# Optimization experiments

Measured on AMD Instinct MI355X. Metric: run time of the kernel, lower is better.

The kernel has to match this reference:

```python
import jax, jax.numpy as jnp
import numpy as np

B, G, D, H, L, MLP = 64, 512, 384, 6, 12, 4
DH = D // H
MASK_RATIO = 0.6
KEEP_RATIO = 0.1
PAD_VAL = -1.0
START_VAL = 1.0
POS_HID = 128
NEG = -1e9


def setup_inputs() -> dict:
    key = jax.random.key(0)
    ks = jax.random.split(key, 24)
    s = 0.02
    inp = {
        "x": jax.random.normal(ks[0], (B, G, D), jnp.float32),
        "center_points": jax.random.normal(ks[1], (B, G, 3), jnp.float32),
        "mask_noise": jax.random.uniform(ks[2], (B, G), jnp.float32),
        # pos embedder MLP: 3 -> 128 -> D
        "pos_w1": jax.random.normal(ks[3], (3, POS_HID), jnp.float32) * s,
        "pos_b1": jnp.zeros((POS_HID,), jnp.float32),
        "pos_w2": jax.random.normal(ks[4], (POS_HID, D), jnp.float32) * s,
        "pos_b2": jnp.zeros((D,), jnp.float32),
        # stacked per-layer transformer params
        "ln1_w": jnp.ones((L, D), jnp.float32),
        "ln1_b": jnp.zeros((L, D), jnp.float32),
        "qkv_w": jax.random.normal(ks[5], (L, D, 3 * D), jnp.float32) * s,
        "qkv_b": jnp.zeros((L, 3 * D), jnp.float32),
        "proj_w": jax.random.normal(ks[6], (L, D, D), jnp.float32) * s,
        "proj_b": jnp.zeros((L, D), jnp.float32),
        "ln2_w": jnp.ones((L, D), jnp.float32),
        "ln2_b": jnp.zeros((L, D), jnp.float32),
        "fc1_w": jax.random.normal(ks[7], (L, D, MLP * D), jnp.float32) * s,
        "fc1_b": jnp.zeros((L, MLP * D), jnp.float32),
        "fc2_w": jax.random.normal(ks[8], (L, MLP * D, D), jnp.float32) * s,
        "fc2_b": jnp.zeros((L, D), jnp.float32),
        # final LayerNorm
        "norm_w": jnp.ones((D,), jnp.float32),
        "norm_b": jnp.zeros((D,), jnp.float32),
    }
    return inp


def _layer_norm(h, w, b, eps=1e-5):
    mu = jnp.mean(h, axis=-1, keepdims=True)
    var = jnp.mean(jnp.square(h - mu), axis=-1, keepdims=True)
    return (h - mu) * jax.lax.rsqrt(var + eps) * w + b


def _random_mask(center, noise):
    # padding tokens: all coords equal PAD_VAL
    pad = jnp.all(center == PAD_VAL, axis=-1)                      # [B, G] bool
    if MASK_RATIO == 0:
        return jnp.zeros(pad.shape, bool), pad
    n = (G - jnp.sum(pad.astype(jnp.int32), axis=-1))              # non-padding count
    k = (n.astype(jnp.float32) * KEEP_RATIO).astype(jnp.int32)     # kept-first tokens
    m = ((n - k).astype(jnp.float32) * MASK_RATIO).astype(jnp.int32)
    M = jnp.max(m)
    j = jnp.arange(G)[None, :]
    # shuffle region [k, n): pick m random slots (uniform subset via rank of noise)
    region = (j >= k[:, None]) & (j < n[:, None])
    u = jnp.where(region, noise, jnp.inf)
    rank = jnp.argsort(jnp.argsort(u, axis=-1), axis=-1)
    shuf = (rank < m[:, None]) & region
    # tail of ones: positions [n, n + M - m)
    tail = (j >= n[:, None]) & (j < (n + M - m)[:, None])
    return shuf | tail, pad


def _attention(h, qw, qb, pw, pb, bias):
    qkv = (h @ qw + qb).reshape(B, G, 3, H, DH).transpose(2, 0, 3, 1, 4)
    q, k, v = qkv[0], qkv[1], qkv[2]                               # [B, H, G, DH]
    s = jnp.einsum('bhqd,bhkd->bhqk', q, k) * (DH ** -0.5) + bias
    a = jax.nn.softmax(s, axis=-1)
    o = jnp.einsum('bhqk,bhkd->bhqd', a, v).transpose(0, 2, 1, 3).reshape(B, G, D)
    return o @ pw + pb


def _forward(x, center_points, mask_noise,
             pos_w1, pos_b1, pos_w2, pos_b2,
             ln1_w, ln1_b, qkv_w, qkv_b, proj_w, proj_b,
             ln2_w, ln2_b, fc1_w, fc1_b, fc2_w, fc2_b,
             norm_w, norm_b):
    # shift right + start token
    start = jnp.full((B, 1, D), START_VAL, x.dtype)
    x = jnp.concatenate([start, x[:, :-1, :]], axis=1)
    # positional embedding of shifted centers + start-token pos
    pos = jax.nn.gelu(center_points[:, :-1, :] @ pos_w1 + pos_b1, approximate=False) @ pos_w2 + pos_b2
    pos = jnp.concatenate([jnp.full((B, 1, D), START_VAL, x.dtype), pos], axis=1)
    # causal | (random column mask & ~eye) attention mask
    triu = jnp.triu(jnp.ones((G, G), bool), 1)
    rand_mask, pad = _random_mask(center_points, mask_noise)
    eye = jnp.eye(G, dtype=bool)
    attn_mask = triu[None, :, :] | (rand_mask[:, None, :] & ~eye[None, :, :])   # [B, G, G]
    bias = jnp.where(attn_mask | pad[:, None, :], NEG, 0.0)[:, None, :, :]      # [B,1,G,G]

    def block(h, p):
        l1w, l1b, qw, qb, pw, pb, l2w, l2b, f1w, f1b, f2w, f2b = p
        h = h + pos
        h = h + _attention(_layer_norm(h, l1w, l1b), qw, qb, pw, pb, bias)
        h = h + (jax.nn.gelu(_layer_norm(h, l2w, l2b) @ f1w + f1b, approximate=False) @ f2w + f2b)
        return h, None

    x, _ = jax.lax.scan(block, x, (ln1_w, ln1_b, qkv_w, qkv_b, proj_w, proj_b,
                                   ln2_w, ln2_b, fc1_w, fc1_b, fc2_w, fc2_b))
    x = _layer_norm(x, norm_w, norm_b)
    return x, pad, attn_mask


def reference(x, center_points, mask_noise,
              pos_w1, pos_b1, pos_w2, pos_b2,
              ln1_w, ln1_b, qkv_w, qkv_b, proj_w, proj_b,
              ln2_w, ln2_b, fc1_w, fc1_b, fc2_w, fc2_b,
              norm_w, norm_b):
    out, pad, attn_mask = _forward(x, center_points, mask_noise,
                                   pos_w1, pos_b1, pos_w2, pos_b2,
                                   ln1_w, ln1_b, qkv_w, qkv_b, proj_w, proj_b,
                                   ln2_w, ln2_b, fc1_w, fc1_b, fc2_w, fc2_b,
                                   norm_w, norm_b)
    # torch repeat_interleave over heads -> [B*H, G, G]
    return out, pad, jnp.repeat(attn_mask, H, axis=0)
```

## Files before the change

### kernel.cpp

```cpp
#include <hip/hip_runtime.h>
#include <math.h>

typedef _Float16 f16;
typedef f16 f16x8 __attribute__((ext_vector_type(8)));
typedef float f32x4 __attribute__((ext_vector_type(4)));

#define NB 64
#define NG 512
#define ND 384
#define NH 6
#define NL 12
#define NDH 64
#define BG (NB * NG)
#define BGD (BG * ND)

#define OFF_WQKV   0
#define OFF_WPROJ  2654208
#define OFF_WFC1   3538944
#define OFF_WFC2   7077888
#define OFF_FLAGS  10616832
#define OFF_NKM    10625024
#define OFF_MMAX   10625216
#define OFF_POS    10625280
#define OFF_HID    23208192
#define OFF_Y      27402496
#define OFF_YBIG   33693952
#define OFF_QB     58859776
#define OFF_KB     65151232
#define OFF_VT     71442688
#define OFF_OB     77734144
#define OFF_W2T    84025600

typedef __attribute__((address_space(3))) void lds_t;
typedef const __attribute__((address_space(1))) void gmem_t;
__device__ __forceinline__ void gload16(const void* g, void* l)
{
    __builtin_amdgcn_global_load_lds((gmem_t*)g, (lds_t*)l, 16, 0, 0);
}

__global__ __launch_bounds__(256)
void transpose_kernel(const float* __restrict__ src, f16* __restrict__ dst,
                      int K, int N)
{
    __shared__ float tile[32][33];
    const int l = blockIdx.z;
    const float* S = src + (size_t)l * K * N;
    f16* D = dst + (size_t)l * K * N;
    const int n0 = blockIdx.x * 32, k0 = blockIdx.y * 32;
    const int tx = threadIdx.x, ty = threadIdx.y;
#pragma unroll
    for (int i = 0; i < 32; i += 8)
        tile[ty + i][tx] = S[(size_t)(k0 + ty + i) * N + n0 + tx];
    __syncthreads();
#pragma unroll
    for (int i = 0; i < 32; i += 8)
        D[(size_t)(n0 + ty + i) * K + k0 + tx] = (f16)tile[tx][ty + i];
}

__global__ __launch_bounds__(256)
void dpos_a(const float* cen, const float* w1, const float* b1, f16* hid)
{
    const int idx = blockIdx.x * 256 + threadIdx.x;
    if (idx >= BG * 128) return;
    const int t = idx >> 7, k = idx & 127;
    const int g = t & (NG - 1);
    if (g == 0) { hid[idx] = (f16)0.f; return; }
    const float* c = cen + (size_t)(t - 1) * 3;
    const float hv = c[0] * w1[k] + c[1] * w1[128 + k] + c[2] * w1[256 + k] + b1[k];
    hid[idx] = (f16)(0.5f * hv * (1.0f + erff(hv * 0.70710678118654752f)));
}

__global__ __launch_bounds__(384)
void pos_fix(float* pos)
{
    const int b = blockIdx.x;
    pos[((size_t)b * NG) * ND + threadIdx.x] = 1.0f;
}

__global__ __launch_bounds__(512)
void dmask_a(const float* cen, float* pad_out, int* nkm)
{
    const int b = blockIdx.x, j = threadIdx.x;
    const float* c = cen + ((size_t)b * NG + j) * 3;
    const bool pad = (c[0] == -1.f) && (c[1] == -1.f) && (c[2] == -1.f);
    pad_out[b * NG + j] = pad ? 1.f : 0.f;
    if (j == 0) {
        int cnt = 0;
        for (int i = 0; i < NG; i++) {
            const float* ci = cen + ((size_t)b * NG + i) * 3;
            cnt += (ci[0] == -1.f && ci[1] == -1.f && ci[2] == -1.f) ? 1 : 0;
        }
        const int n = NG - cnt;
        const int k = (int)((float)n * 0.1f);
        const int m = (int)((float)(n - k) * 0.6f);
        nkm[b * 3] = n; nkm[b * 3 + 1] = k; nkm[b * 3 + 2] = m;
    }
}

__global__ void dmask_m(const int* nkm, int* Mmax)
{
    if (threadIdx.x == 0 && blockIdx.x == 0) {
        int M = 0;
        for (int b = 0; b < NB; b++) M = max(M, nkm[b * 3 + 2]);
        *Mmax = M;
    }
}

__global__ __launch_bounds__(512)
void dmask_b(const float* cen, const float* noi, const int* nkm,
             const int* Mmax, unsigned char* flags)
{
    const int b = blockIdx.x, j = threadIdx.x;
    const int n = nkm[b * 3], k = nkm[b * 3 + 1], m = nkm[b * 3 + 2];
    const int M = *Mmax;
    const float nz = noi[b * NG + j];
    const bool inreg = (j >= k) && (j < n);
    bool shuf = false;
    if (inreg) {
        int cnt = 0;
        for (int i = 0; i < NG; i++) {
            if (i < k || i >= n) continue;
            const float ui = noi[b * NG + i];
            cnt += (ui < nz) || (ui == nz && i < j);
        }
        shuf = cnt < m;
    }
    const float* c = cen + ((size_t)b * NG + j) * 3;
    const bool pad = (c[0] == -1.f) && (c[1] == -1.f) && (c[2] == -1.f);
    const bool tail = (j >= n) && (j < n + M - m);
    flags[b * NG + j] = (unsigned char)(((shuf | tail) ? 1 : 0) | (pad ? 2 : 0));
}

__global__ __launch_bounds__(512)
void flags_rep_kernel(const unsigned char* flags, float* mo)
{
    const int bq = blockIdx.x;
    const int b = bq >> 9, q = bq & (NG - 1);
    const int j = threadIdx.x;
    mo[(((size_t)(b * NH) * NG + q) * NG) + j] = (float)flags[b * NG + j];
}

__global__ __launch_bounds__(512)
void mask_out_kernel(float* mo)
{
    const int bq = blockIdx.x;
    const int b = bq >> 9, q = bq & (NG - 1);
    const int j = threadIdx.x;
    const unsigned char f =
        (unsigned char)mo[(((size_t)(b * NH) * NG + q) * NG) + j];
    const float val = ((q < j) || ((f & 1) && (q != j))) ? 1.0f : 0.0f;
#pragma unroll
    for (int h = 0; h < NH; h++)
        mo[(((size_t)(b * NH + h) * NG + q) * NG) + j] = val;
}

__global__ __launch_bounds__(256)
void h0_kernel(const float* x, float* h)
{
    const size_t i = (size_t)blockIdx.x * 256 + threadIdx.x;
    const int g = (int)((i / ND) & (NG - 1));
    const float xv = x[(g == 0) ? i : (i - ND)];
    h[i] = (g == 0) ? 1.0f : xv;
}

template<int MODE>
__global__ __launch_bounds__(256)
void lnb_kernel(float* __restrict__ h, const float* __restrict__ pos,
                const float* __restrict__ w, const float* __restrict__ bb,
                f16* __restrict__ y16, float* __restrict__ y32)
{
    __shared__ float red[4][64];
    const int wid = threadIdx.x >> 6;
    const int lane = threadIdx.x & 63;
    const int t = blockIdx.x * 4 + wid;
    const size_t base = (size_t)t * ND + lane;
    float v[6];
    float s = 0.f;
#pragma unroll
    for (int i = 0; i < 6; i++) {
        float xv = h[base + i * 64];
        if constexpr (MODE == 0) xv += pos[base + i * 64];
        v[i] = xv; s += xv;
    }
    if constexpr (MODE == 0) {
#pragma unroll
        for (int i = 0; i < 6; i++) h[base + i * 64] = v[i];
    }
    red[wid][lane] = s;
    __syncthreads();
    for (int st = 32; st > 0; st >>= 1) {
        if (lane < st) red[wid][lane] += red[wid][lane + st];
        __syncthreads();
    }
    const float mu = red[wid][0] * (1.f / ND);
    float vs = 0.f;
#pragma unroll
    for (int i = 0; i < 6; i++) { const float d = v[i] - mu; vs += d * d; }
    __syncthreads();
    red[wid][lane] = vs;
    __syncthreads();
    for (int st = 32; st > 0; st >>= 1) {
        if (lane < st) red[wid][lane] += red[wid][lane + st];
        __syncthreads();
    }
    const float rstd = rsqrtf(red[wid][0] * (1.f / ND) + 1e-5f);
#pragma unroll
    for (int i = 0; i < 6; i++) {
        const float o = (v[i] - mu) * rstd * w[lane + i * 64] + bb[lane + i * 64];
        if constexpr (MODE == 2) y32[base + i * 64] = o;
        else                     y16[base + i * 64] = (f16)o;
    }
}

template<int MODE>
__global__ __launch_bounds__(256)
void gemm_kernel(const f16* __restrict__ A, const f16* __restrict__ Bt,
                 const float* __restrict__ bias, int K, int NT,
                 float* __restrict__ hbuf, f16* __restrict__ out16,
                 f16* __restrict__ Qo, f16* __restrict__ Ko, f16* __restrict__ Vo)
{
    __shared__ f16 sA[128 * 64];
    __shared__ f16 sB[128 * 64];
    const int tid = threadIdx.x;
    const int w = tid >> 6, lane = tid & 63;
    const int lr = lane & 15, lg = lane >> 4;
    const int wm = w >> 1, wn = w & 1;
    const int N = NT * 128;

    const int nwg = gridDim.x;
    const int chunk = nwg >> 3;
    const int flat = (blockIdx.x & 7) * chunk + (blockIdx.x >> 3);
    const int m0 = (flat / NT) * 128;
    const int n0 = (flat % NT) * 128;

    f32x4 acc[4][4];
#pragma unroll
    for (int mf = 0; mf < 4; mf++)
#pragma unroll
        for (int nf = 0; nf < 4; nf++)
            acc[mf][nf] = (f32x4){0.f, 0.f, 0.f, 0.f};

    const int srow0 = w * 8 + (lane >> 3);
    const int scolB = (lane & 7) * 16;

    for (int k0 = 0; k0 < K; k0 += 64) {
        __syncthreads();
#pragma unroll
        for (int i = 0; i < 4; i++) {
            const int row = i * 32 + srow0;
            const int colB = scolB ^ ((row & 7) << 4);
            const char* ga = (const char*)(A + (size_t)(m0 + row) * K + k0) + colB;
            const char* gb = (const char*)(Bt + (size_t)(n0 + row) * K + k0) + colB;
            gload16(ga, (char*)sA + row * 128 + scolB);
            gload16(gb, (char*)sB + row * 128 + scolB);
        }
        __syncthreads();
#pragma unroll
        for (int kk = 0; kk < 64; kk += 32) {
            f16x8 af[4], bf[4];
#pragma unroll
            for (int mf = 0; mf < 4; mf++) {
                const int r = wm * 64 + mf * 16 + lr;
                const int cb = ((kk + lg * 8) * 2) ^ ((r & 7) << 4);
                af[mf] = *(const f16x8*)((const char*)sA + r * 128 + cb);
            }
#pragma unroll
            for (int nf = 0; nf < 4; nf++) {
                const int r = wn * 64 + nf * 16 + lr;
                const int cb = ((kk + lg * 8) * 2) ^ ((r & 7) << 4);
                bf[nf] = *(const f16x8*)((const char*)sB + r * 128 + cb);
            }
#pragma unroll
            for (int mf = 0; mf < 4; mf++)
#pragma unroll
                for (int nf = 0; nf < 4; nf++)
                    acc[mf][nf] = __builtin_amdgcn_mfma_f32_16x16x32_f16(
                        af[mf], bf[nf], acc[mf][nf], 0, 0, 0);
        }
    }

#pragma unroll
    for (int mf = 0; mf < 4; mf++) {
#pragma unroll
        for (int nf = 0; nf < 4; nf++) {
            const int n_g = n0 + wn * 64 + nf * 16 + lr;
            const float bv = bias[n_g];
#pragma unroll
            for (int r = 0; r < 4; r++) {
                const int m_g = m0 + wm * 64 + mf * 16 + lg * 4 + r;
                const float v = acc[mf][nf][r] + bv;
                if constexpr (MODE == 1) {
                    hbuf[(size_t)m_g * N + n_g] += v;
                } else if constexpr (MODE == 2) {
                    const float ge = 0.5f * v * (1.0f + erff(v * 0.70710678118654752f));
                    out16[(size_t)m_g * N + n_g] = (f16)ge;
                } else if constexpr (MODE == 3) {
                    hbuf[(size_t)m_g * N + n_g] = v;
                } else {
                    const int which = n_g / ND;
                    const int rem = n_g - which * ND;
                    const int hh = rem >> 6, dh = rem & 63;
                    const int bb2 = m_g >> 9, gg = m_g & (NG - 1);
                    if (which == 0)
                        Qo[((size_t)(bb2 * NH + hh) * NG + gg) * NDH + dh] = (f16)v;
                    else if (which == 1)
                        Ko[((size_t)(bb2 * NH + hh) * NG + gg) * NDH + dh] = (f16)v;
                    else
                        Vo[((size_t)(bb2 * NH + hh) * NDH + dh) * NG + gg] = (f16)v;
                }
            }
        }
    }
}

__global__ __launch_bounds__(256)
void attn_kernel(const f16* __restrict__ Q, const f16* __restrict__ Kt,
                 const f16* __restrict__ V, const unsigned char* __restrict__ flags,
                 f16* __restrict__ O)
{
    __shared__ f16 sQ[128][72];
    __shared__ f16 sK[64][72];
    __shared__ f16 sV[64][72];
    __shared__ f16 sP[4][16][72];
    const int tid = threadIdx.x;
    const int w = tid >> 6, lane = tid & 63;
    const int lr = lane & 15, lg = lane >> 4;
    const int q0 = blockIdx.x * 128;
    const int bh = blockIdx.y;
    const int b = bh / NH, hh = bh - b * NH;
    const f16* Qg = Q + ((size_t)bh * NG + q0) * NDH;
    const f16* Kg = Kt + (size_t)bh * NG * NDH;
    const f16* Vg = V + (size_t)bh * NDH * NG;
    const unsigned char* fl = flags + b * NG;

#pragma unroll
    for (int i = 0; i < 4; i++) {
        const int c = tid + i * 256;
        const int r = c >> 3, cc = (c & 7) * 8;
        *(f16x8*)&sQ[r][cc] = *(const f16x8*)(Qg + r * NDH + cc);
    }
    __syncthreads();
    f16x8 aq[2][2];
#pragma unroll
    for (int hf = 0; hf < 2; hf++) {
        aq[hf][0] = *(const f16x8*)&sQ[hf * 64 + w * 16 + lr][lg * 8];
        aq[hf][1] = *(const f16x8*)&sQ[hf * 64 + w * 16 + lr][32 + lg * 8];
    }

    float m_run[2][4], l_run[2][4];
    f32x4 o[2][4];
#pragma unroll
    for (int hf = 0; hf < 2; hf++)
#pragma unroll
        for (int r = 0; r < 4; r++) {
            m_run[hf][r] = -INFINITY; l_run[hf][r] = 0.f;
            o[hf][r] = (f32x4){0.f, 0.f, 0.f, 0.f};
        }

    const int ntile = 2 * blockIdx.x + 2;
    for (int jt = 0; jt < ntile; jt++) {
        const int j0 = jt * 64;
        __syncthreads();
#pragma unroll
        for (int i = 0; i < 2; i++) {
            const int c = tid + i * 256;
            const int r = c >> 3, cc = (c & 7) * 8;
            *(f16x8*)&sK[r][cc] = *(const f16x8*)(Kg + (size_t)(j0 + r) * NDH + cc);
            *(f16x8*)&sV[r][cc] = *(const f16x8*)(Vg + (size_t)r * NG + j0 + cc);
        }
        __syncthreads();

#pragma unroll
        for (int hf = 0; hf < 2; hf++) {
            if (jt >= ntile - 1 + hf) continue;
            f32x4 s[4];
#pragma unroll
            for (int nf = 0; nf < 4; nf++) s[nf] = (f32x4){0.f, 0.f, 0.f, 0.f};
#pragma unroll
            for (int kf = 0; kf < 2; kf++) {
#pragma unroll
                for (int nf = 0; nf < 4; nf++) {
                    f16x8 bk = *(const f16x8*)&sK[nf * 16 + lr][kf * 32 + lg * 8];
                    s[nf] = __builtin_amdgcn_mfma_f32_16x16x32_f16(aq[hf][kf], bk, s[nf], 0, 0, 0);
                }
            }
#pragma unroll
            for (int nf = 0; nf < 4; nf++) {
                const int j_g = j0 + nf * 16 + lr;
                const unsigned char f = fl[j_g];
#pragma unroll
                for (int r = 0; r < 4; r++) {
                    const int q_g = q0 + hf * 64 + w * 16 + lg * 4 + r;
                    const bool masked = (q_g < j_g) || (f & 2) || ((f & 1) && (j_g != q_g));
                    s[nf][r] = s[nf][r] * 0.125f + (masked ? -1e9f : 0.f);
                }
            }
#pragma unroll
            for (int r = 0; r < 4; r++) {
                float mx = fmaxf(fmaxf(s[0][r], s[1][r]), fmaxf(s[2][r], s[3][r]));
#pragma unroll
                for (int off = 1; off < 16; off <<= 1) mx = fmaxf(mx, __shfl_xor(mx, off));
                const float nm = fmaxf(m_run[hf][r], mx);
                const float sc = __expf(m_run[hf][r] - nm);
                m_run[hf][r] = nm;
                l_run[hf][r] *= sc;
#pragma unroll
                for (int nf = 0; nf < 4; nf++) o[hf][nf][r] *= sc;
                float ls = 0.f;
#pragma unroll
                for (int nf = 0; nf < 4; nf++) {
                    const float p = __expf(s[nf][r] - nm);
                    ls += p;
                    sP[w][lg * 4 + r][nf * 16 + lr] = (f16)p;
                }
                l_run[hf][r] += ls;
            }
#pragma unroll
            for (int kf = 0; kf < 2; kf++) {
                f16x8 ap = *(const f16x8*)&sP[w][lr][kf * 32 + lg * 8];
#pragma unroll
                for (int nf = 0; nf < 4; nf++) {
                    f16x8 bv = *(const f16x8*)&sV[nf * 16 + lr][kf * 32 + lg * 8];
                    o[hf][nf] = __builtin_amdgcn_mfma_f32_16x16x32_f16(ap, bv, o[hf][nf], 0, 0, 0);
                }
            }
        }
    }

#pragma unroll
    for (int hf = 0; hf < 2; hf++) {
        float inv[4];
#pragma unroll
        for (int r = 0; r < 4; r++) {
            float l = l_run[hf][r];
#pragma unroll
            for (int off = 1; off < 16; off <<= 1) l += __shfl_xor(l, off);
            inv[r] = 1.f / l;
        }
#pragma unroll
        for (int nf = 0; nf < 4; nf++) {
#pragma unroll
            for (int r = 0; r < 4; r++) {
                const int q_g = q0 + hf * 64 + w * 16 + lg * 4 + r;
                const int dh = nf * 16 + lr;
                O[((size_t)(b * NG + q_g)) * ND + hh * NDH + dh] = (f16)(o[hf][nf][r] * inv[r]);
            }
        }
    }
}

extern "C" void kernel_launch(void* const* d_in, const int* in_sizes, int n_in,
                              void* d_out, int out_size, void* d_ws, size_t ws_size,
                              hipStream_t stream)
{
    (void)d_ws; (void)ws_size;

    static const int exp_sizes[21] = {
        12582912, 98304, 32768,
        384, 128, 49152, 384,
        4608, 4608,
        5308416, 13824,
        1769472, 4608,
        4608, 4608,
        7077888, 18432,
        7077888, 4608,
        384, 384
    };
    if (n_in != 21 || out_size != 113278976) return;
    for (int i = 0; i < 21; i++) if (in_sizes[i] != exp_sizes[i]) return;

    const float* x    = (const float*)d_in[0];
    const float* cen  = (const float*)d_in[1];
    const float* noi  = (const float*)d_in[2];
    const float* pw1  = (const float*)d_in[3];
    const float* pb1  = (const float*)d_in[4];
    const float* pw2  = (const float*)d_in[5];
    const float* pb2  = (const float*)d_in[6];
    const float* ln1w = (const float*)d_in[7];
    const float* ln1b = (const float*)d_in[8];
    const float* qkvw = (const float*)d_in[9];
    const float* qkvb = (const float*)d_in[10];
    const float* projw= (const float*)d_in[11];
    const float* projb= (const float*)d_in[12];
    const float* ln2w = (const float*)d_in[13];
    const float* ln2b = (const float*)d_in[14];
    const float* fc1w = (const float*)d_in[15];
    const float* fc1b = (const float*)d_in[16];
    const float* fc2w = (const float*)d_in[17];
    const float* fc2b = (const float*)d_in[18];
    const float* nw   = (const float*)d_in[19];
    const float* nb   = (const float*)d_in[20];

    float* out0    = (float*)d_out;
    float* pad_out = out0 + BGD;
    float* R       = pad_out + BG;

    float* Hb   = out0;
    f16* WqkvT  = (f16*)(R + OFF_WQKV);
    f16* WprojT = (f16*)(R + OFF_WPROJ);
    f16* Wfc1T  = (f16*)(R + OFF_WFC1);
    f16* Wfc2T  = (f16*)(R + OFF_WFC2);
    unsigned char* flags = (unsigned char*)(R + OFF_FLAGS);
    int* nkm  = (int*)(R + OFF_NKM);
    int* Mmax = (int*)(R + OFF_MMAX);
    float* POS = R + OFF_POS;
    f16* HID   = (f16*)(R + OFF_HID);
    f16* Y     = (f16*)(R + OFF_Y);
    f16* Ybig  = (f16*)(R + OFF_YBIG);
    f16* Qb    = (f16*)(R + OFF_QB);
    f16* Kb    = (f16*)(R + OFF_KB);
    f16* Vt    = (f16*)(R + OFF_VT);
    f16* Ob    = (f16*)(R + OFF_OB);
    f16* W2T   = (f16*)(R + OFF_W2T);

    dim3 tb(32, 8);
    transpose_kernel<<<dim3(36, 12, NL), tb, 0, stream>>>(qkvw, WqkvT, 384, 1152);
    transpose_kernel<<<dim3(12, 12, NL), tb, 0, stream>>>(projw, WprojT, 384, 384);
    transpose_kernel<<<dim3(48, 12, NL), tb, 0, stream>>>(fc1w, Wfc1T, 384, 1536);
    transpose_kernel<<<dim3(12, 48, NL), tb, 0, stream>>>(fc2w, Wfc2T, 1536, 384);
    transpose_kernel<<<dim3(12, 4, 1),  tb, 0, stream>>>(pw2, W2T, 128, 384);

    dmask_a<<<NB, 512, 0, stream>>>(cen, pad_out, nkm);
    dmask_m<<<1, 64, 0, stream>>>(nkm, Mmax);
    dmask_b<<<NB, 512, 0, stream>>>(cen, noi, nkm, Mmax, flags);
    dpos_a<<<BG * 128 / 256, 256, 0, stream>>>(cen, pw1, pb1, HID);
    gemm_kernel<3><<<768, 256, 0, stream>>>(HID, W2T, pb2, 128, 3,
                                            POS, nullptr, nullptr, nullptr, nullptr);
    pos_fix<<<NB, 384, 0, stream>>>(POS);
    h0_kernel<<<BGD / 256, 256, 0, stream>>>(x, Hb);

    for (int l = 0; l < NL; l++) {
        lnb_kernel<0><<<BG / 4, 256, 0, stream>>>(Hb, POS, ln1w + l * ND, ln1b + l * ND, Y, nullptr);
        gemm_kernel<0><<<2304, 256, 0, stream>>>(Y, WqkvT + (size_t)l * 442368,
                                                 qkvb + l * 1152, 384, 9,
                                                 nullptr, nullptr, Qb, Kb, Vt);
        attn_kernel<<<dim3(4, NB * NH), 256, 0, stream>>>(Qb, Kb, Vt, flags, Ob);
        gemm_kernel<1><<<768, 256, 0, stream>>>(Ob, WprojT + (size_t)l * 147456,
                                                projb + l * ND, 384, 3,
                                                Hb, nullptr, nullptr, nullptr, nullptr);
        lnb_kernel<1><<<BG / 4, 256, 0, stream>>>(Hb, nullptr, ln2w + l * ND, ln2b + l * ND, Y, nullptr);
        gemm_kernel<2><<<3072, 256, 0, stream>>>(Y, Wfc1T + (size_t)l * 589824,
                                                 fc1b + l * 1536, 384, 12,
                                                 nullptr, Ybig, nullptr, nullptr, nullptr);
        gemm_kernel<1><<<768, 256, 0, stream>>>(Ybig, Wfc2T + (size_t)l * 589824,
                                                fc2b + l * ND, 1536, 3,
                                                Hb, nullptr, nullptr, nullptr, nullptr);
    }

    lnb_kernel<2><<<BG / 4, 256, 0, stream>>>(Hb, nullptr, nw, nb, nullptr, out0);
    flags_rep_kernel<<<BG, 512, 0, stream>>>(flags, R);
    mask_out_kernel<<<BG, 512, 0, stream>>>(R);
}
```

Baseline: 5.288 ms.

## Store residual stream in fp16 and fuse pos-add into fc2 epilogue

Keeps the residual hidden state in fp16 instead of fp32, which halves the read-modify-write traffic in the residual GEMM epilogues and the LayerNorm reads. The next layer's positional-embedding add moves out of the LN1 kernel into the fc2 epilogue through a new MODE 4, and h0 pre-adds pos for layer 0. The LN1 kernel therefore no longer writes back the hidden state. The trade-off is that accumulating the residual in fp16 across 12 layers loses precision and can push the output past tolerance.

```diff
diff --git a/kernel.cpp b/kernel.cpp
--- a/kernel.cpp
+++ b/kernel.cpp
@@ -23,13 +23,14 @@
 #define OFF_MMAX   10625216
 #define OFF_POS    10625280
 #define OFF_HID    23208192
-#define OFF_Y      27402496
-#define OFF_YBIG   33693952
-#define OFF_QB     58859776
-#define OFF_KB     65151232
-#define OFF_VT     71442688
-#define OFF_OB     77734144
-#define OFF_W2T    84025600
+#define OFF_Y      25305344
+#define OFF_YBIG   31596800
+#define OFF_QB     56762624
+#define OFF_KB     63054080
+#define OFF_VT     69345536
+#define OFF_OB     75636992
+#define OFF_W2T    81928448
+#define OFF_HB     81953024
 
 typedef __attribute__((address_space(3))) void lds_t;
 typedef const __attribute__((address_space(1))) void gmem_t;
@@ -155,17 +156,18 @@
 }
 
 __global__ __launch_bounds__(256)
-void h0_kernel(const float* x, float* h)
+void h0_kernel(const float* x, const float* pos, f16* h)
 {
     const size_t i = (size_t)blockIdx.x * 256 + threadIdx.x;
     const int g = (int)((i / ND) & (NG - 1));
     const float xv = x[(g == 0) ? i : (i - ND)];
-    h[i] = (g == 0) ? 1.0f : xv;
+    const float base = (g == 0) ? 1.0f : xv;
+    h[i] = (f16)(base + pos[i]);
 }
 
 template<int MODE>
 __global__ __launch_bounds__(256)
-void lnb_kernel(float* __restrict__ h, const float* __restrict__ pos,
+void lnb_kernel(const f16* __restrict__ h,
                 const float* __restrict__ w, const float* __restrict__ bb,
                 f16* __restrict__ y16, float* __restrict__ y32)
 {
@@ -178,13 +180,8 @@
     float s = 0.f;
 #pragma unroll
     for (int i = 0; i < 6; i++) {
-        float xv = h[base + i * 64];
-        if constexpr (MODE == 0) xv += pos[base + i * 64];
+        const float xv = (float)h[base + i * 64];
         v[i] = xv; s += xv;
-    }
-    if constexpr (MODE == 0) {
-#pragma unroll
-        for (int i = 0; i < 6; i++) h[base + i * 64] = v[i];
     }
     red[wid][lane] = s;
     __syncthreads();
@@ -216,7 +213,8 @@
 __global__ __launch_bounds__(256)
 void gemm_kernel(const f16* __restrict__ A, const f16* __restrict__ Bt,
                  const float* __restrict__ bias, int K, int NT,
-                 float* __restrict__ hbuf, f16* __restrict__ out16,
+                 f16* __restrict__ hres, const float* __restrict__ posadd,
+                 float* __restrict__ out32, f16* __restrict__ out16,
                  f16* __restrict__ Qo, f16* __restrict__ Ko, f16* __restrict__ Vo)
 {
     __shared__ f16 sA[128 * 64];
@@ -289,13 +287,16 @@
             for (int r = 0; r < 4; r++) {
                 const int m_g = m0 + wm * 64 + mf * 16 + lg * 4 + r;
                 const float v = acc[mf][nf][r] + bv;
+                const size_t oidx = (size_t)m_g * N + n_g;
                 if constexpr (MODE == 1) {
-                    hbuf[(size_t)m_g * N + n_g] += v;
+                    hres[oidx] = (f16)((float)hres[oidx] + v);
+                } else if constexpr (MODE == 4) {
+                    hres[oidx] = (f16)((float)hres[oidx] + v + posadd[oidx]);
                 } else if constexpr (MODE == 2) {
                     const float ge = 0.5f * v * (1.0f + erff(v * 0.70710678118654752f));
-                    out16[(size_t)m_g * N + n_g] = (f16)ge;
+                    out16[oidx] = (f16)ge;
                 } else if constexpr (MODE == 3) {
-                    hbuf[(size_t)m_g * N + n_g] = v;
+                    out32[oidx] = v;
                 } else {
                     const int which = n_g / ND;
                     const int rem = n_g - which * ND;
@@ -495,7 +496,6 @@
     float* pad_out = out0 + BGD;
     float* R       = pad_out + BG;
 
-    float* Hb   = out0;
     f16* WqkvT  = (f16*)(R + OFF_WQKV);
     f16* WprojT = (f16*)(R + OFF_WPROJ);
     f16* Wfc1T  = (f16*)(R + OFF_WFC1);
@@ -512,6 +512,7 @@
     f16* Vt    = (f16*)(R + OFF_VT);
     f16* Ob    = (f16*)(R + OFF_OB);
     f16* W2T   = (f16*)(R + OFF_W2T);
+    f16* Hb    = (f16*)(R + OFF_HB);
 
     dim3 tb(32, 8);
     transpose_kernel<<<dim3(36, 12, NL), tb, 0, stream>>>(qkvw, WqkvT, 384, 1152);
@@ -525,29 +526,41 @@
     dmask_b<<<NB, 512, 0, stream>>>(cen, noi, nkm, Mmax, flags);
     dpos_a<<<BG * 128 / 256, 256, 0, stream>>>(cen, pw1, pb1, HID);
     gemm_kernel<3><<<768, 256, 0, stream>>>(HID, W2T, pb2, 128, 3,
-                                            POS, nullptr, nullptr, nullptr, nullptr);
+                                            nullptr, nullptr, POS, nullptr,
+                                            nullptr, nullptr, nullptr);
     pos_fix<<<NB, 384, 0, stream>>>(POS);
-    h0_kernel<<<BGD / 256, 256, 0, stream>>>(x, Hb);
+    h0_kernel<<<BGD / 256, 256, 0, stream>>>(x, POS, Hb);
 
     for (int l = 0; l < NL; l++) {
-        lnb_kernel<0><<<BG / 4, 256, 0, stream>>>(Hb, POS, ln1w + l * ND, ln1b + l * ND, Y, nullptr);
+        lnb_kernel<1><<<BG / 4, 256, 0, stream>>>(Hb, ln1w + l * ND, ln1b + l * ND, Y, nullptr);
         gemm_kernel<0><<<2304, 256, 0, stream>>>(Y, WqkvT + (size_t)l * 442368,
                                                  qkvb + l * 1152, 384, 9,
-                                                 nullptr, nullptr, Qb, Kb, Vt);
+                                                 nullptr, nullptr, nullptr, nullptr,
+                                                 Qb, Kb, Vt);
         attn_kernel<<<dim3(4, NB * NH), 256, 0, stream>>>(Qb, Kb, Vt, flags, Ob);
         gemm_kernel<1><<<768, 256, 0, stream>>>(Ob, WprojT + (size_t)l * 147456,
                                                 projb + l * ND, 384, 3,
-                                                Hb, nullptr, nullptr, nullptr, nullptr);
-        lnb_kernel<1><<<BG / 4, 256, 0, stream>>>(Hb, nullptr, ln2w + l * ND, ln2b + l * ND, Y, nullptr);
+                                                Hb, nullptr, nullptr, nullptr,
+                                                nullptr, nullptr, nullptr);
+        lnb_kernel<1><<<BG / 4, 256, 0, stream>>>(Hb, ln2w + l * ND, ln2b + l * ND, Y, nullptr);
         gemm_kernel<2><<<3072, 256, 0, stream>>>(Y, Wfc1T + (size_t)l * 589824,
                                                  fc1b + l * 1536, 384, 12,
-                                                 nullptr, Ybig, nullptr, nullptr, nullptr);
-        gemm_kernel<1><<<768, 256, 0, stream>>>(Ybig, Wfc2T + (size_t)l * 589824,
-                                                fc2b + l * ND, 1536, 3,
-                                                Hb, nullptr, nullptr, nullptr, nullptr);
-    }
-
-    lnb_kernel<2><<<BG / 4, 256, 0, stream>>>(Hb, nullptr, nw, nb, nullptr, out0);
+                                                 nullptr, nullptr, nullptr, Ybig,
+                                                 nullptr, nullptr, nullptr);
+        if (l < NL - 1) {
+            gemm_kernel<4><<<768, 256, 0, stream>>>(Ybig, Wfc2T + (size_t)l * 589824,
+                                                    fc2b + l * ND, 1536, 3,
+                                                    Hb, POS, nullptr, nullptr,
+                                                    nullptr, nullptr, nullptr);
+        } else {
+            gemm_kernel<1><<<768, 256, 0, stream>>>(Ybig, Wfc2T + (size_t)l * 589824,
+                                                    fc2b + l * ND, 1536, 3,
+                                                    Hb, nullptr, nullptr, nullptr,
+                                                    nullptr, nullptr, nullptr);
+        }
+    }
+
+    lnb_kernel<2><<<BG / 4, 256, 0, stream>>>(Hb, nw, nb, nullptr, out0);
     flags_rep_kernel<<<BG, 512, 0, stream>>>(flags, R);
     mask_out_kernel<<<BG, 512, 0, stream>>>(R);
 }
```

Result: faster. 5.074 ms (-4.1%).
